# Optimization experiments

Measured on AMD Instinct MI355X. Metric: run time of the kernel, lower is better.

The kernel has to match this reference:

```python
import jax, jax.numpy as jnp
import numpy as np

D_MODEL = 1024
B, T_Q, T_KV = 4, 2048, 2048


def _linear_params(key, d_in, d_out):
    kw, kb = jax.random.split(key)
    W = jax.random.normal(kw, (d_out, d_in), dtype=jnp.float32) * 0.02
    b = jax.random.normal(kb, (d_out,), dtype=jnp.float32) * 0.02
    return W, b


def setup_inputs() -> dict:
    key = jax.random.key(0)
    ks = jax.random.split(key, 7)
    latent_space = jax.random.normal(ks[0], (B, T_Q, D_MODEL), dtype=jnp.float32)
    input_space = jax.random.normal(ks[1], (B, T_KV, D_MODEL), dtype=jnp.float32)
    Wl, bl = _linear_params(ks[2], D_MODEL, D_MODEL)
    Wu, bu = _linear_params(ks[3], D_MODEL, D_MODEL)
    WA, bA = _linear_params(ks[4], D_MODEL, D_MODEL)  # A_proj: d -> J (J = d)
    WV, bV = _linear_params(ks[5], D_MODEL, D_MODEL)  # V_proj: J -> d
    Wo, bo = _linear_params(ks[6], D_MODEL, D_MODEL)
    return {
        "latent_space": latent_space, "input_space": input_space,
        "Wl": Wl, "bl": bl, "Wu": Wu, "bu": bu,
        "WA": WA, "bA": bA, "WV": WV, "bV": bV,
        "Wo": Wo, "bo": bo,
    }


def reference(latent_space, input_space, Wl, bl, Wu, bu, WA, bA, WV, bV, Wo, bo):
    # emb_0 = l_proj(latent)            [B, T_q, d]
    emb0 = jnp.einsum('bqd,ed->bqe', latent_space, Wl) + bl
    # l = softmax(u_proj(emb_0), -1)^T  [B, d, T_q]
    l = jax.nn.softmax(jnp.einsum('bqd,ed->bqe', emb0, Wu) + bu, axis=-1)
    l = jnp.swapaxes(l, -2, -1)
    # D = A_proj(input)                 [B, T_kv, J]
    Dm = jnp.einsum('bkd,jd->bkj', input_space, WA) + bA
    # A = softmax(V_proj(D), dim=-2)    softmax over T_kv
    A = jax.nn.softmax(jnp.einsum('bkj,dj->bkd', Dm, WV) + bV, axis=-2)
    # w = A @ l                         [B, T_kv, T_q]
    w = jnp.einsum('bkd,bdq->bkq', A, l)
    # o = w @ o_proj(latent)            [B, T_kv, d]
    ov = jnp.einsum('bqd,ed->bqe', latent_space, Wo) + bo
    o = jnp.einsum('bkq,bqd->bkd', w, ov)
    return o
```

## Files before the change

### kernel.cpp

```cpp
#include <hip/hip_runtime.h>
#include <hip/hip_bf16.h>
#include <stdint.h>

typedef __attribute__((ext_vector_type(8))) short bf16x8;
typedef __attribute__((ext_vector_type(4))) float f32x4;
typedef __attribute__((ext_vector_type(4))) unsigned short u16x4;

#define B_  4
#define T_  2048
#define D_  1024
#define BM  128
#define BN  128
#define BK  32

__device__ __forceinline__ float bf2f(ushort u) {
  union { unsigned int i; float f; } v; v.i = ((unsigned int)u) << 16; return v.f;
}
__device__ __forceinline__ ushort f2bf(float f) {
  return (ushort)(__bfloat16_as_ushort(__float2bfloat16(f)));
}
__device__ __forceinline__ void async16(const void* g, void* l) {
  __builtin_amdgcn_global_load_lds(
      (const __attribute__((address_space(1))) void*)g,
      (__attribute__((address_space(3))) void*)l, 16, 0, 0);
}
__device__ __forceinline__ int swz4(int r) { return (r ^ (r >> 2)) & 3; }

__global__ __launch_bounds__(256)
void prep(const float* __restrict__ lat, const float* __restrict__ inp,
          const float* __restrict__ Wl, const float* __restrict__ bl,
          const float* __restrict__ Wu, const float* __restrict__ bu,
          const float* __restrict__ WA, const float* __restrict__ bA,
          const float* __restrict__ WV, const float* __restrict__ bV,
          const float* __restrict__ Wo, const float* __restrict__ bo,
          ushort* __restrict__ xBf, ushort* __restrict__ xBf2,
          ushort* __restrict__ w1, ushort* __restrict__ w2,
          ushort* __restrict__ wCatWo, float* __restrict__ bc, float* __restrict__ bc2)
{
  __shared__ alignas(16) ushort t[64 * 65];
  const long NW = (long)D_ * D_;
  const int bx = blockIdx.x;
  const int tid = threadIdx.x;
  if (bx < 16384) {
    const float* in = bx < 8192 ? lat : inp;
    ushort* out = bx < 8192 ? xBf : xBf2;
    const long i = (long)(bx & 8191) * 256 + tid;
    const float4 v = *(const float4*)(in + i * 4);
    u16x4 o;
    o[0] = f2bf(v.x); o[1] = f2bf(v.y); o[2] = f2bf(v.z); o[3] = f2bf(v.w);
    *(u16x4*)(out + i * 4) = o;
  } else if (bx < 19456) {
    const int seg = (bx - 16384) >> 10;
    const float* in  = seg == 0 ? Wu : (seg == 1 ? WV : Wo);
    ushort* out = seg == 0 ? w1 : (seg == 1 ? w1 + NW : wCatWo);
    const long i = (long)((bx - 16384) & 1023) * 256 + tid;
    const float4 v = *(const float4*)(in + i * 4);
    u16x4 o;
    o[0] = f2bf(v.x); o[1] = f2bf(v.y); o[2] = f2bf(v.z); o[3] = f2bf(v.w);
    *(u16x4*)(out + i * 4) = o;
  } else if (bx < 19968) {
    const int z = (bx - 19456) >> 8;
    const int w = (bx - 19456) & 255;
    const float* in = z ? WA : Wl;
    ushort* out = z ? w2 + NW : w2;
    const int c0 = (w & 15) * 64, r0 = (w >> 4) * 64;
    const int tx = tid & 15, ty = tid >> 4;
#pragma unroll
    for (int i = 0; i < 4; ++i) {
      const int r = ty + i * 16;
      const float4 v = *(const float4*)(in + (long)(r0 + r) * D_ + c0 + tx * 4);
      t[(tx * 4 + 0) * 65 + r] = f2bf(v.x);
      t[(tx * 4 + 1) * 65 + r] = f2bf(v.y);
      t[(tx * 4 + 2) * 65 + r] = f2bf(v.z);
      t[(tx * 4 + 3) * 65 + r] = f2bf(v.w);
    }
    __syncthreads();
#pragma unroll
    for (int i = 0; i < 4; ++i) {
      const int c = ty + i * 16;
      u16x4 v;
#pragma unroll
      for (int j = 0; j < 4; ++j) v[j] = t[c * 65 + tx * 4 + j];
      *(u16x4*)(out + (long)(c0 + c) * D_ + r0 + tx * 4) = v;
    }
  } else {
    const int z = (bx - 19968) >> 8;
    const int w = (bx - 19968) & 255;
    const float* W    = z ? WV : Wu;
    const float* bin  = z ? bA : bl;
    const float* badd = z ? bV : bu;
    float* out        = z ? bc2 : bc;
    const int wv = tid >> 6, lane = tid & 63;
    const int e = w * 4 + wv;
    const float* row = W + (long)e * D_;
    float s = 0.f;
#pragma unroll
    for (int i = 0; i < 16; ++i) s += row[lane + i * 64] * bin[lane + i * 64];
#pragma unroll
    for (int off = 32; off; off >>= 1) s += __shfl_xor(s, off);
    if (lane == 0) out[e] = s + badd[e];
  }
}

template<bool OUT_F32, bool HAS_BIAS, bool EXP_OUT>
__global__ __launch_bounds__(256, 2)
void gemm_nt(const ushort* __restrict__ A, const ushort* __restrict__ B,
             const float* __restrict__ bias, void* __restrict__ C,
             int N, int K, long sA, long sB, long sC)
{
  __shared__ alignas(16) ushort As[BM * BK];
  __shared__ alignas(16) ushort Bs[BN * BK];
  const int tid  = threadIdx.x;
  const int wave = tid >> 6;
  const int lane = tid & 63;
  const int wm   = wave >> 1;
  const int wn   = wave & 1;
  const int bz   = blockIdx.z;
  const int tileN = blockIdx.x * BN;
  const int tileM = blockIdx.y * BM;
  A += (long)bz * sA;
  B += (long)bz * sB;

  const int lrow   = lane >> 2;
  const int lchunk = (lane & 3) ^ swz4(lrow);

  f32x4 acc[4][4];
#pragma unroll
  for (int i = 0; i < 4; ++i)
#pragma unroll
    for (int j = 0; j < 4; ++j) acc[i][j] = (f32x4){0.f, 0.f, 0.f, 0.f};

  const int frow = lane & 15;
  const int kg   = lane >> 4;
  const int coff = ((kg ^ swz4(frow)) << 3);

  for (int kt = 0; kt < K; kt += BK) {
    __syncthreads();
#pragma unroll
    for (int i = 0; i < 2; ++i) {
      const int rg  = wave * 2 + i;
      const int row = rg * 16 + lrow;
      async16(A + (long)(tileM + row) * K + kt + lchunk * 8, (void*)(As + rg * 16 * BK));
      async16(B + (long)(tileN + row) * K + kt + lchunk * 8, (void*)(Bs + rg * 16 * BK));
    }
    __syncthreads();
    bf16x8 af[4], bfr[4];
#pragma unroll
    for (int mi = 0; mi < 4; ++mi)
      af[mi] = *(const bf16x8*)(As + (wm * 64 + mi * 16 + frow) * BK + coff);
#pragma unroll
    for (int ni = 0; ni < 4; ++ni)
      bfr[ni] = *(const bf16x8*)(Bs + (wn * 64 + ni * 16 + frow) * BK + coff);
#pragma unroll
    for (int mi = 0; mi < 4; ++mi)
#pragma unroll
      for (int ni = 0; ni < 4; ++ni)
        acc[mi][ni] = __builtin_amdgcn_mfma_f32_16x16x32_bf16(af[mi], bfr[ni], acc[mi][ni], 0, 0, 0);
  }

  const int rowbase = tileM + wm * 64 + ((lane >> 4) << 2);
  const int colbase = tileN + wn * 64 + (lane & 15);
#pragma unroll
  for (int ni = 0; ni < 4; ++ni) {
    const int col = colbase + ni * 16;
    float bv = 0.f;
    if constexpr (HAS_BIAS) bv = bias[col];
#pragma unroll
    for (int mi = 0; mi < 4; ++mi) {
#pragma unroll
      for (int r = 0; r < 4; ++r) {
        const int row = rowbase + mi * 16 + r;
        float v = acc[mi][ni][r] + bv;
        if constexpr (EXP_OUT) v = __expf(v);
        const long idx = (long)bz * sC + (long)row * N + col;
        if constexpr (OUT_F32) ((float*)C)[idx] = v;
        else ((ushort*)C)[idx] = f2bf(v);
      }
    }
  }
}

#define PH_SYNC_IN()                                               \
  __builtin_amdgcn_s_barrier();                                    \
  asm volatile("s_waitcnt lgkmcnt(0)" ::: "memory");               \
  __builtin_amdgcn_sched_barrier(0);                               \
  __builtin_amdgcn_s_setprio(1)
#define PH_SYNC_OUT()                                              \
  __builtin_amdgcn_s_setprio(0);                                   \
  __builtin_amdgcn_s_barrier()

__global__ __launch_bounds__(512, 2)
void gemm256(const ushort* __restrict__ A, const ushort* __restrict__ Bm,
             const float* __restrict__ bias1, const float* __restrict__ bias2,
             ushort* __restrict__ C1, ushort* __restrict__ C2,
             int ldA, int ldB)
{
  __shared__ alignas(16) ushort AbS[2 * 16384];
  __shared__ alignas(16) ushort BbS[2 * 16384];

  const int gx = gridDim.x;
  const int nwg = gx * gridDim.y;
  int fid = blockIdx.y * gx + blockIdx.x;
  fid = (fid & 7) * (nwg >> 3) + (fid >> 3);
  const int bx = fid % gx;
  const int by = fid / gx;
  const int tileM = by * 256, tileN = bx * 256;

  const int tid  = threadIdx.x;
  const int wid  = tid >> 6;
  const int lane = tid & 63;
  const int wm   = wid >> 2;
  const int wn   = wid & 3;

  const int srow = tid >> 2;
  const int sc   = (((tid & 3) ^ ((tid >> 3) & 3)) << 3);
  const ushort* gA0 = A  + (long)(tileM + srow) * ldA + sc;
  const ushort* gA1 = A  + (long)(tileM + 128 + srow) * ldA + sc;
  const ushort* gB0 = Bm + (long)(tileN + srow) * ldB + sc;
  const ushort* gB1 = Bm + (long)(tileN + 128 + srow) * ldB + sc;
  const int dofs = tid << 3;

#define STA(b, kh, t) { \
    async16(gA0 + (long)(t) * 64 + (kh) * 32, AbS + (b) * 16384 + (kh) * 8192 + dofs); \
    async16(gA1 + (long)(t) * 64 + (kh) * 32, AbS + (b) * 16384 + (kh) * 8192 + 4096 + dofs); }
#define STB(b, kh, t) { \
    async16(gB0 + (long)(t) * 64 + (kh) * 32, BbS + (b) * 16384 + (kh) * 8192 + dofs); \
    async16(gB1 + (long)(t) * 64 + (kh) * 32, BbS + (b) * 16384 + (kh) * 8192 + 4096 + dofs); }

  const int frow = lane & 15;
  const int cofs = (((lane >> 4) ^ ((frow >> 1) & 3)) << 3);
  int aoff[8], boff[4];
#pragma unroll
  for (int mi = 0; mi < 8; ++mi)
    aoff[mi] = wm * 4096 + (mi * 16 + frow) * 32 + cofs;
#pragma unroll
  for (int n = 0; n < 4; ++n) {
    const int Brow = wn * 64 + n * 16 + frow;
    boff[n] = (Brow >> 7) * 4096 + (Brow & 127) * 32 + cofs;
  }

  f32x4 acc[8][4];
#pragma unroll
  for (int i = 0; i < 8; ++i)
#pragma unroll
    for (int j = 0; j < 4; ++j) acc[i][j] = (f32x4){0.f, 0.f, 0.f, 0.f};

  STA(0, 0, 0); STB(0, 0, 0);
  STA(0, 1, 0); STB(0, 1, 0);
  STA(1, 0, 1); STB(1, 0, 1);
  asm volatile("s_waitcnt vmcnt(8)" ::: "memory");
  __builtin_amdgcn_s_barrier();

#pragma unroll 1
  for (int t = 0; t < 16; ++t) {
    const int buf = t & 1;
    const ushort* Ac = AbS + buf * 16384;
    const ushort* Bc = BbS + buf * 16384;
    bf16x8 fa[4], fb[4], ga[4];

#pragma unroll
    for (int n = 0; n < 4; ++n) fb[n] = *(const bf16x8*)(Bc + boff[n]);
#pragma unroll
    for (int m = 0; m < 4; ++m) fa[m] = *(const bf16x8*)(Ac + aoff[m]);
    if (t <= 14) { STA(buf ^ 1, 1, t + 1); STB(buf ^ 1, 1, t + 1); }
    PH_SYNC_IN();
#pragma unroll
    for (int m = 0; m < 4; ++m)
#pragma unroll
      for (int n = 0; n < 4; ++n)
        acc[m][n] = __builtin_amdgcn_mfma_f32_16x16x32_bf16(fa[m], fb[n], acc[m][n], 0, 0, 0);
    PH_SYNC_OUT();

#pragma unroll
    for (int m = 0; m < 4; ++m) ga[m] = *(const bf16x8*)(Ac + aoff[4 + m]);
    if (t <= 14) asm volatile("s_waitcnt vmcnt(8)" ::: "memory");
    else         asm volatile("s_waitcnt vmcnt(0)" ::: "memory");
    PH_SYNC_IN();
#pragma unroll
    for (int m = 0; m < 4; ++m)
#pragma unroll
      for (int n = 0; n < 4; ++n)
        acc[4 + m][n] = __builtin_amdgcn_mfma_f32_16x16x32_bf16(ga[m], fb[n], acc[4 + m][n], 0, 0, 0);
    PH_SYNC_OUT();

#pragma unroll
    for (int n = 0; n < 4; ++n) fb[n] = *(const bf16x8*)(Bc + boff[n] + 8192);
#pragma unroll
    for (int m = 0; m < 4; ++m) fa[m] = *(const bf16x8*)(Ac + aoff[m] + 8192);
    if (t <= 13) { STA(buf, 0, t + 2); STB(buf, 0, t + 2); }
    PH_SYNC_IN();
#pragma unroll
    for (int m = 0; m < 4; ++m)
#pragma unroll
      for (int n = 0; n < 4; ++n)
        acc[m][n] = __builtin_amdgcn_mfma_f32_16x16x32_bf16(fa[m], fb[n], acc[m][n], 0, 0, 0);
    PH_SYNC_OUT();

#pragma unroll
    for (int m = 0; m < 4; ++m) ga[m] = *(const bf16x8*)(Ac + aoff[4 + m] + 8192);
    if (t <= 13)      asm volatile("s_waitcnt vmcnt(8)" ::: "memory");
    else if (t == 14) asm volatile("s_waitcnt vmcnt(4)" ::: "memory");
    PH_SYNC_IN();
#pragma unroll
    for (int m = 0; m < 4; ++m)
#pragma unroll
      for (int n = 0; n < 4; ++n)
        acc[4 + m][n] = __builtin_amdgcn_mfma_f32_16x16x32_bf16(ga[m], fb[n], acc[4 + m][n], 0, 0, 0);
    PH_SYNC_OUT();
  }
#undef STA
#undef STB

  const bool second = tileN >= 1024;
  ushort* Cp = second ? C2 : C1;
  const float* bb = second ? bias2 : bias1;
  const int cb = tileN - (second ? 1024 : 0) + wn * 64 + (lane & 15);
  const int rb = tileM + wm * 128 + ((lane >> 4) << 2);
#pragma unroll
  for (int mi = 0; mi < 8; ++mi) {
    const int mrow = rb + mi * 16;
#pragma unroll
    for (int ni = 0; ni < 4; ++ni) {
      const int col = cb + ni * 16;
      const float bv = bb[col];
#pragma unroll
      for (int r = 0; r < 4; ++r)
        Cp[(long)(mrow + r) * 1024 + col] = f2bf(acc[mi][ni][r] + bv);
    }
  }
}

template<int MODE>
__global__ __launch_bounds__(512, 2)
void gemm128(const ushort* __restrict__ A, const ushort* __restrict__ Bm,
             const float* __restrict__ bias1, void* __restrict__ C1,
             int ldA, int ldB, long sAz, long sBz, long sCz)
{
  __shared__ alignas(16) ushort AbS[2 * 16384];
  __shared__ alignas(16) ushort BbS[2 * 8192];

  const int gx = gridDim.x, gy = gridDim.y;
  const int nwg = gx * gy * gridDim.z;
  int fid = (blockIdx.z * gy + blockIdx.y) * gx + blockIdx.x;
  fid = (fid & 7) * (nwg >> 3) + (fid >> 3);
  const int bx = fid % gx;
  const int by = (fid / gx) % gy;
  const int bz = fid / (gx * gy);
  const int tileM = by * 256, tileN = bx * 128;

  const ushort* Ap = A;
  const ushort* Bp = Bm;
  if constexpr (MODE == 2) {
    Ap += (long)(bz >> 1) * sAz + (long)(bz & 1) * 1024;
    Bp += (long)(bz >> 1) * sBz + (long)(bz & 1) * 1024;
  } else {
    Ap += (long)bz * sAz;
    Bp += (long)bz * sBz;
  }

  const int tid  = threadIdx.x;
  const int wid  = tid >> 6;
  const int lane = tid & 63;
  const int wm   = wid >> 1;
  const int wn   = wid & 1;

  const int srow = tid >> 2;
  const int sc   = (((tid & 3) ^ ((tid >> 3) & 3)) << 3);
  const ushort* gA0 = Ap + (long)(tileM + srow) * ldA + sc;
  const ushort* gA1 = Ap + (long)(tileM + 128 + srow) * ldA + sc;
  const ushort* gB0 = Bp + (long)(tileN + srow) * ldB + sc;
  const int dofs = tid << 3;

#define STA(b, kh, t) { \
    async16(gA0 + (long)(t) * 64 + (kh) * 32, AbS + (b) * 16384 + (kh) * 8192 + dofs); \
    async16(gA1 + (long)(t) * 64 + (kh) * 32, AbS + (b) * 16384 + (kh) * 8192 + 4096 + dofs); }
#define STB(b, kh, t) \
    async16(gB0 + (long)(t) * 64 + (kh) * 32, BbS + (b) * 8192 + (kh) * 4096 + dofs);

  const int frow = lane & 15;
  const int cofs = (((lane >> 4) ^ ((frow >> 1) & 3)) << 3);
  int aoff[4], boff[4];
#pragma unroll
  for (int mi = 0; mi < 4; ++mi) {
    const int R = wm * 64 + mi * 16 + frow;
    aoff[mi] = (R >> 7) * 4096 + (R & 127) * 32 + cofs;
  }
#pragma unroll
  for (int n = 0; n < 4; ++n)
    boff[n] = (wn * 64 + n * 16 + frow) * 32 + cofs;

  f32x4 acc[4][4];
#pragma unroll
  for (int i = 0; i < 4; ++i)
#pragma unroll
    for (int j = 0; j < 4; ++j) acc[i][j] = (f32x4){0.f, 0.f, 0.f, 0.f};

  STA(0, 0, 0); STB(0, 0, 0);
  STA(0, 1, 0); STB(0, 1, 0);
  STA(1, 0, 1); STB(1, 0, 1);
  asm volatile("s_waitcnt vmcnt(6)" ::: "memory");
  __builtin_amdgcn_s_barrier();

#pragma unroll 1
  for (int t = 0; t < 16; ++t) {
    const int buf = t & 1;
    const ushort* Ac = AbS + buf * 16384;
    const ushort* Bc = BbS + buf * 8192;
    bf16x8 fa[4], fb[4];

#pragma unroll
    for (int n = 0; n < 4; ++n) fb[n] = *(const bf16x8*)(Bc + boff[n]);
#pragma unroll
    for (int m = 0; m < 4; ++m) fa[m] = *(const bf16x8*)(Ac + aoff[m]);
    if (t <= 14) { STA(buf ^ 1, 1, t + 1); STB(buf ^ 1, 1, t + 1); }
    if (t <= 14) asm volatile("s_waitcnt vmcnt(6)" ::: "memory");
    else         asm volatile("s_waitcnt vmcnt(0)" ::: "memory");
    PH_SYNC_IN();
#pragma unroll
    for (int m = 0; m < 4; ++m)
#pragma unroll
      for (int n = 0; n < 4; ++n)
        acc[m][n] = __builtin_amdgcn_mfma_f32_16x16x32_bf16(fa[m], fb[n], acc[m][n], 0, 0, 0);
    PH_SYNC_OUT();

#pragma unroll
    for (int n = 0; n < 4; ++n) fb[n] = *(const bf16x8*)(Bc + boff[n] + 4096);
#pragma unroll
    for (int m = 0; m < 4; ++m) fa[m] = *(const bf16x8*)(Ac + aoff[m] + 8192);
    if (t <= 13) { STA(buf, 0, t + 2); STB(buf, 0, t + 2); }
    if (t <= 13)      asm volatile("s_waitcnt vmcnt(6)" ::: "memory");
    else if (t == 14) asm volatile("s_waitcnt vmcnt(3)" ::: "memory");
    PH_SYNC_IN();
#pragma unroll
    for (int m = 0; m < 4; ++m)
#pragma unroll
      for (int n = 0; n < 4; ++n)
        acc[m][n] = __builtin_amdgcn_mfma_f32_16x16x32_bf16(fa[m], fb[n], acc[m][n], 0, 0, 0);
    PH_SYNC_OUT();
  }
#undef STA
#undef STB

  const int cb = tileN + wn * 64 + (lane & 15);
  const int rb = tileM + wm * 64 + ((lane >> 4) << 2);

  if constexpr (MODE == 1) {
    ushort* Cp = (ushort*)C1;
#pragma unroll
    for (int ni = 0; ni < 4; ++ni) {
      const int col = cb + ni * 16;
      const float bv = bias1[col];
#pragma unroll
      for (int mi = 0; mi < 4; ++mi)
#pragma unroll
        for (int r = 0; r < 4; ++r)
          Cp[(long)(rb + mi * 16 + r) * 1024 + col] = f2bf(__expf(acc[mi][ni][r] + bv));
    }
  } else if constexpr (MODE == 2) {
    ushort* Cp = (ushort*)C1 + ((long)(bz & 1) * B_ + (bz >> 1)) * ((long)D_ * D_);
#pragma unroll
    for (int ni = 0; ni < 4; ++ni) {
      const int col = cb + ni * 16;
#pragma unroll
      for (int mi = 0; mi < 4; ++mi)
#pragma unroll
        for (int r = 0; r < 4; ++r)
          Cp[(long)(rb + mi * 16 + r) * 1024 + col] = f2bf(acc[mi][ni][r]);
    }
  } else {
    float* Cp = (float*)C1 + (long)bz * sCz;
#pragma unroll
    for (int ni = 0; ni < 4; ++ni) {
      const int col = cb + ni * 16;
#pragma unroll
      for (int mi = 0; mi < 4; ++mi)
#pragma unroll
        for (int r = 0; r < 4; ++r)
          Cp[(long)(rb + mi * 16 + r) * 1024 + col] = acc[mi][ni][r];
    }
  }
}

__global__ __launch_bounds__(256)
void reduce2_scale(const ushort* __restrict__ P, const float* __restrict__ cinv,
                   ushort* __restrict__ MT)
{
  const long stride = (long)B_ * D_ * D_;
  const long base = ((long)blockIdx.x * 256 + threadIdx.x) * 8;
  const int b = (int)(base >> 20);
  const int e0 = (int)(base & (D_ - 1));
  bf16x8 p0 = *(const bf16x8*)(P + base);
  bf16x8 p1 = *(const bf16x8*)(P + stride + base);
  const float4 c0 = *(const float4*)(cinv + (long)b * D_ + e0);
  const float4 c1 = *(const float4*)(cinv + (long)b * D_ + e0 + 4);
  const float cc[8] = {c0.x, c0.y, c0.z, c0.w, c1.x, c1.y, c1.z, c1.w};
  bf16x8 o;
#pragma unroll
  for (int j = 0; j < 8; ++j)
    o[j] = (short)f2bf((bf2f((ushort)p0[j]) + bf2f((ushort)p1[j])) * cc[j]);
  *(bf16x8*)(MT + base) = o;
}

__global__ __launch_bounds__(256)
void softmax_row(ushort* __restrict__ S)
{
  const long base = (long)blockIdx.x * D_;
  const int tid = threadIdx.x;
  float e[4], s = 0.f;
#pragma unroll
  for (int i = 0; i < 4; ++i) { e[i] = __expf(bf2f(S[base + i * 256 + tid])); s += e[i]; }
#pragma unroll
  for (int off = 32; off; off >>= 1) s += __shfl_xor(s, off);
  __shared__ float reds[4];
  if ((tid & 63) == 0) reds[tid >> 6] = s;
  __syncthreads();
  s = reds[0] + reds[1] + reds[2] + reds[3];
  const float inv = 1.f / s;
#pragma unroll
  for (int i = 0; i < 4; ++i)
    S[base + i * 256 + tid] = f2bf(e[i] * inv);
}

__global__ __launch_bounds__(256)
void transpose2(const ushort* __restrict__ l, ushort* __restrict__ lT,
                const ushort* __restrict__ ov, ushort* __restrict__ ovT)
{
  __shared__ alignas(16) ushort t[64 * 65];
  const int z = blockIdx.z;
  const int b = z & (B_ - 1);
  const ushort* in = (z < B_ ? l : ov) + (long)b * T_ * D_;
  ushort* out      = (z < B_ ? lT : ovT) + (long)b * (long)D_ * T_;
  const int c0 = blockIdx.x * 64, r0 = blockIdx.y * 64;
  const int tx = threadIdx.x & 15, ty = threadIdx.x >> 4;
#pragma unroll
  for (int i = 0; i < 4; ++i) {
    const int r = ty + i * 16;
    u16x4 v = *(const u16x4*)(in + (long)(r0 + r) * D_ + c0 + tx * 4);
#pragma unroll
    for (int c = 0; c < 4; ++c) t[(tx * 4 + c) * 65 + r] = v[c];
  }
  __syncthreads();
#pragma unroll
  for (int i = 0; i < 4; ++i) {
    const int c = ty + i * 16;
    u16x4 v;
#pragma unroll
    for (int j = 0; j < 4; ++j) v[j] = t[c * 65 + tx * 4 + j];
    *(u16x4*)(out + (long)(c0 + c) * T_ + r0 + tx * 4) = v;
  }
}

__global__ __launch_bounds__(256)
void colsum_part(const ushort* __restrict__ E, float* __restrict__ psum)
{
  const int d = blockIdx.x * 256 + threadIdx.x;
  const int c = blockIdx.y;
  const int b = blockIdx.z;
  const ushort* p = E + ((long)b * T_ + (long)c * 128) * D_ + d;
  float s = 0.f;
#pragma unroll 4
  for (int r = 0; r < 128; ++r) s += bf2f(p[(long)r * D_]);
  psum[((long)b * 16 + c) * D_ + d] = s;
}

__global__ __launch_bounds__(256)
void colsum_comb(const float* __restrict__ psum, float* __restrict__ cinv)
{
  const int d = blockIdx.x * 256 + threadIdx.x;
  const int b = blockIdx.y;
  float s = 0.f;
#pragma unroll
  for (int c = 0; c < 16; ++c) s += psum[((long)b * 16 + c) * D_ + d];
  cinv[(long)b * D_ + d] = 1.f / s;
}

extern "C" void kernel_launch(void* const* d_in, const int* in_sizes, int n_in,
                              void* d_out, int out_size, void* d_ws, size_t ws_size,
                              hipStream_t stream)
{
  (void)in_sizes; (void)n_in; (void)out_size; (void)ws_size;
  const float* lat = (const float*)d_in[0];
  const float* inp = (const float*)d_in[1];
  const float* Wl  = (const float*)d_in[2];
  const float* bl  = (const float*)d_in[3];
  const float* Wu  = (const float*)d_in[4];
  const float* bu  = (const float*)d_in[5];
  const float* WA  = (const float*)d_in[6];
  const float* bA  = (const float*)d_in[7];
  const float* WV  = (const float*)d_in[8];
  const float* bV  = (const float*)d_in[9];
  const float* Wo  = (const float*)d_in[10];
  const float* bo  = (const float*)d_in[11];

  char* w = (char*)d_ws;
  auto carve = [&](size_t bytes) { char* p = w; w += (bytes + 255) & ~(size_t)255; return p; };
  const long NT = (long)B_ * T_ * D_;
  const long NW = (long)D_ * D_;
  ushort* xBf   = (ushort*)carve(NT * 2);
  ushort* xBf2  = (ushort*)carve(NT * 2);
  ushort* bufA  = (ushort*)carve(NT * 2);
  ushort* bufB  = (ushort*)carve(NT * 2);
  ushort* scr   = (ushort*)carve(NT * 2);
  ushort* MT    = (ushort*)carve((long)B_ * NW * 2);
  ushort* wCat  = (ushort*)carve(3 * NW * 2);
  float*  bc    = (float*)carve(D_ * 4);
  float*  bc2   = (float*)carve(D_ * 4);
  float*  psum  = (float*)carve(64 * 1024 * 4);
  float*  cinv  = (float*)carve(8 * 1024 * 4);
  ushort* w1 = scr;
  ushort* w2 = scr + 2 * NW;
  ushort* ovT = scr;
  ushort* part = bufB;

  const dim3 blk(256, 1, 1);
  const dim3 blk5(512, 1, 1);

  prep<<<dim3(20480), blk, 0, stream>>>(lat, inp, Wl, bl, Wu, bu, WA, bA, WV, bV, Wo, bo,
                                        xBf, xBf2, w1, w2, wCat + NW, bc, bc2);
  gemm_nt<false, false, false><<<dim3(8, 8, 2), blk, 0, stream>>>(
      w1, w2, nullptr, wCat, D_, D_, NW, NW, 2 * NW);
  gemm256<<<dim3(8, 32, 1), blk5, 0, stream>>>(
      xBf, wCat, bc, bo, bufB, bufA, D_, D_);
  softmax_row<<<dim3(B_ * T_), blk, 0, stream>>>(bufB);
  transpose2<<<dim3(16, 32, 2 * B_), blk, 0, stream>>>(bufB, xBf, bufA, ovT);
  gemm128<2><<<dim3(8, 4, 8), blk5, 0, stream>>>(
      ovT, xBf, nullptr, part, T_, T_, (long)D_ * T_, (long)D_ * T_, 0);
  gemm128<1><<<dim3(8, 32, 1), blk5, 0, stream>>>(
      xBf2, wCat + 2 * NW, bc2, bufA, D_, D_, 0, 0, 0);
  colsum_part<<<dim3(4, 16, B_), blk, 0, stream>>>(bufA, psum);
  colsum_comb<<<dim3(4, B_, 1), blk, 0, stream>>>(psum, cinv);
  reduce2_scale<<<dim3(2048), blk, 0, stream>>>(part, cinv, MT);
  gemm128<3><<<dim3(8, 8, 4), blk5, 0, stream>>>(
      bufA, MT, nullptr, d_out, D_, D_,
      (long)T_ * D_, NW, (long)T_ * D_);
}
```

Baseline: 321.2 us.

## Use BK=64 swizzled tiles with triple-buffered LDS pipelines and drop gemm_nt

Both pipelined GEMM kernels now load full 64-wide K tiles per row with an 8-way XOR swizzle instead of two 32-wide halves. Their LDS buffering moves to a triple-buffer rotation (B only in gemm256, A and B in gemm128), so prefetches are issued two tiles ahead and spread across the phases. The old simple gemm_nt used for weight fusion is replaced by a new MODE 0 of the pipelined gemm128. This is meant to improve global-load width and latency hiding, at the cost of more LDS per block, which may lower occupancy.

```diff
diff --git a/kernel.cpp b/kernel.cpp
--- a/kernel.cpp
+++ b/kernel.cpp
@@ -9,9 +9,6 @@
 #define B_  4
 #define T_  2048
 #define D_  1024
-#define BM  128
-#define BN  128
-#define BK  32
 
 __device__ __forceinline__ float bf2f(ushort u) {
   union { unsigned int i; float f; } v; v.i = ((unsigned int)u) << 16; return v.f;
@@ -24,7 +21,6 @@
       (const __attribute__((address_space(1))) void*)g,
       (__attribute__((address_space(3))) void*)l, 16, 0, 0);
 }
-__device__ __forceinline__ int swz4(int r) { return (r ^ (r >> 2)) & 3; }
 
 __global__ __launch_bounds__(256)
 void prep(const float* __restrict__ lat, const float* __restrict__ inp,
@@ -102,84 +98,6 @@
   }
 }
 
-template<bool OUT_F32, bool HAS_BIAS, bool EXP_OUT>
-__global__ __launch_bounds__(256, 2)
-void gemm_nt(const ushort* __restrict__ A, const ushort* __restrict__ B,
-             const float* __restrict__ bias, void* __restrict__ C,
-             int N, int K, long sA, long sB, long sC)
-{
-  __shared__ alignas(16) ushort As[BM * BK];
-  __shared__ alignas(16) ushort Bs[BN * BK];
-  const int tid  = threadIdx.x;
-  const int wave = tid >> 6;
-  const int lane = tid & 63;
-  const int wm   = wave >> 1;
-  const int wn   = wave & 1;
-  const int bz   = blockIdx.z;
-  const int tileN = blockIdx.x * BN;
-  const int tileM = blockIdx.y * BM;
-  A += (long)bz * sA;
-  B += (long)bz * sB;
-
-  const int lrow   = lane >> 2;
-  const int lchunk = (lane & 3) ^ swz4(lrow);
-
-  f32x4 acc[4][4];
-#pragma unroll
-  for (int i = 0; i < 4; ++i)
-#pragma unroll
-    for (int j = 0; j < 4; ++j) acc[i][j] = (f32x4){0.f, 0.f, 0.f, 0.f};
-
-  const int frow = lane & 15;
-  const int kg   = lane >> 4;
-  const int coff = ((kg ^ swz4(frow)) << 3);
-
-  for (int kt = 0; kt < K; kt += BK) {
-    __syncthreads();
-#pragma unroll
-    for (int i = 0; i < 2; ++i) {
-      const int rg  = wave * 2 + i;
-      const int row = rg * 16 + lrow;
-      async16(A + (long)(tileM + row) * K + kt + lchunk * 8, (void*)(As + rg * 16 * BK));
-      async16(B + (long)(tileN + row) * K + kt + lchunk * 8, (void*)(Bs + rg * 16 * BK));
-    }
-    __syncthreads();
-    bf16x8 af[4], bfr[4];
-#pragma unroll
-    for (int mi = 0; mi < 4; ++mi)
-      af[mi] = *(const bf16x8*)(As + (wm * 64 + mi * 16 + frow) * BK + coff);
-#pragma unroll
-    for (int ni = 0; ni < 4; ++ni)
-      bfr[ni] = *(const bf16x8*)(Bs + (wn * 64 + ni * 16 + frow) * BK + coff);
-#pragma unroll
-    for (int mi = 0; mi < 4; ++mi)
-#pragma unroll
-      for (int ni = 0; ni < 4; ++ni)
-        acc[mi][ni] = __builtin_amdgcn_mfma_f32_16x16x32_bf16(af[mi], bfr[ni], acc[mi][ni], 0, 0, 0);
-  }
-
-  const int rowbase = tileM + wm * 64 + ((lane >> 4) << 2);
-  const int colbase = tileN + wn * 64 + (lane & 15);
-#pragma unroll
-  for (int ni = 0; ni < 4; ++ni) {
-    const int col = colbase + ni * 16;
-    float bv = 0.f;
-    if constexpr (HAS_BIAS) bv = bias[col];
-#pragma unroll
-    for (int mi = 0; mi < 4; ++mi) {
-#pragma unroll
-      for (int r = 0; r < 4; ++r) {
-        const int row = rowbase + mi * 16 + r;
-        float v = acc[mi][ni][r] + bv;
-        if constexpr (EXP_OUT) v = __expf(v);
-        const long idx = (long)bz * sC + (long)row * N + col;
-        if constexpr (OUT_F32) ((float*)C)[idx] = v;
-        else ((ushort*)C)[idx] = f2bf(v);
-      }
-    }
-  }
-}
-
 #define PH_SYNC_IN()                                               \
   __builtin_amdgcn_s_barrier();                                    \
   asm volatile("s_waitcnt lgkmcnt(0)" ::: "memory");               \
@@ -189,6 +107,7 @@
   __builtin_amdgcn_s_setprio(0);                                   \
   __builtin_amdgcn_s_barrier()
 
+
 __global__ __launch_bounds__(512, 2)
 void gemm256(const ushort* __restrict__ A, const ushort* __restrict__ Bm,
              const float* __restrict__ bias1, const float* __restrict__ bias2,
@@ -196,7 +115,7 @@
              int ldA, int ldB)
 {
   __shared__ alignas(16) ushort AbS[2 * 16384];
-  __shared__ alignas(16) ushort BbS[2 * 16384];
+  __shared__ alignas(16) ushort BbS[3 * 16384];
 
   const int gx = gridDim.x;
   const int nwg = gx * gridDim.y;
@@ -212,32 +131,26 @@
   const int wm   = wid >> 2;
   const int wn   = wid & 3;
 
-  const int srow = tid >> 2;
-  const int sc   = (((tid & 3) ^ ((tid >> 3) & 3)) << 3);
-  const ushort* gA0 = A  + (long)(tileM + srow) * ldA + sc;
-  const ushort* gA1 = A  + (long)(tileM + 128 + srow) * ldA + sc;
-  const ushort* gB0 = Bm + (long)(tileN + srow) * ldB + sc;
-  const ushort* gB1 = Bm + (long)(tileN + 128 + srow) * ldB + sc;
-  const int dofs = tid << 3;
-
-#define STA(b, kh, t) { \
-    async16(gA0 + (long)(t) * 64 + (kh) * 32, AbS + (b) * 16384 + (kh) * 8192 + dofs); \
-    async16(gA1 + (long)(t) * 64 + (kh) * 32, AbS + (b) * 16384 + (kh) * 8192 + 4096 + dofs); }
-#define STB(b, kh, t) { \
-    async16(gB0 + (long)(t) * 64 + (kh) * 32, BbS + (b) * 16384 + (kh) * 8192 + dofs); \
-    async16(gB1 + (long)(t) * 64 + (kh) * 32, BbS + (b) * 16384 + (kh) * 8192 + 4096 + dofs); }
+  const int srow8 = tid >> 3;
+  const int scol8 = ((tid & 7) ^ (srow8 & 7)) << 3;
+  const ushort* gAs = A  + (long)(tileM + srow8) * ldA + scol8;
+  const ushort* gBs = Bm + (long)(tileN + srow8) * ldB + scol8;
+  const int sdst = tid << 3;
+
+#define STA(b, i, t) async16(gAs + (long)((i) * 64) * ldA + (t) * 64, \
+                             AbS + (b) * 16384 + (i) * 4096 + sdst)
+#define STB(b, i, t) async16(gBs + (long)((i) * 64) * ldB + (t) * 64, \
+                             BbS + (b) * 16384 + (i) * 4096 + sdst)
 
   const int frow = lane & 15;
-  const int cofs = (((lane >> 4) ^ ((frow >> 1) & 3)) << 3);
-  int aoff[8], boff[4];
-#pragma unroll
-  for (int mi = 0; mi < 8; ++mi)
-    aoff[mi] = wm * 4096 + (mi * 16 + frow) * 32 + cofs;
-#pragma unroll
-  for (int n = 0; n < 4; ++n) {
-    const int Brow = wn * 64 + n * 16 + frow;
-    boff[n] = (Brow >> 7) * 4096 + (Brow & 127) * 32 + cofs;
-  }
+  const int kg   = lane >> 4;
+  const int ck0 = ((kg       ^ (frow & 7)) << 3);
+  const int ck1 = (((4 + kg) ^ (frow & 7)) << 3);
+  int aoffr[8], boffr[4];
+#pragma unroll
+  for (int mi = 0; mi < 8; ++mi) aoffr[mi] = (wm * 128 + mi * 16 + frow) * 64;
+#pragma unroll
+  for (int n = 0; n < 4; ++n)    boffr[n]  = (wn * 64 + n * 16 + frow) * 64;
 
   f32x4 acc[8][4];
 #pragma unroll
@@ -245,24 +158,32 @@
 #pragma unroll
     for (int j = 0; j < 4; ++j) acc[i][j] = (f32x4){0.f, 0.f, 0.f, 0.f};
 
-  STA(0, 0, 0); STB(0, 0, 0);
-  STA(0, 1, 0); STB(0, 1, 0);
-  STA(1, 0, 1); STB(1, 0, 1);
+#pragma unroll
+  for (int i = 0; i < 4; ++i) STA(0, i, 0);
+#pragma unroll
+  for (int i = 0; i < 4; ++i) STB(0, i, 0);
+#pragma unroll
+  for (int i = 0; i < 4; ++i) STA(1, i, 1);
+#pragma unroll
+  for (int i = 0; i < 4; ++i) STB(1, i, 1);
   asm volatile("s_waitcnt vmcnt(8)" ::: "memory");
   __builtin_amdgcn_s_barrier();
 
 #pragma unroll 1
   for (int t = 0; t < 16; ++t) {
     const int buf = t & 1;
+    const int bB  = t - (t / 3) * 3;
+    const int nA  = (t + 1) & 1;
+    const int nB  = (t + 2) - ((t + 2) / 3) * 3;
     const ushort* Ac = AbS + buf * 16384;
-    const ushort* Bc = BbS + buf * 16384;
+    const ushort* Bc = BbS + bB * 16384;
     bf16x8 fa[4], fb[4], ga[4];
 
 #pragma unroll
-    for (int n = 0; n < 4; ++n) fb[n] = *(const bf16x8*)(Bc + boff[n]);
-#pragma unroll
-    for (int m = 0; m < 4; ++m) fa[m] = *(const bf16x8*)(Ac + aoff[m]);
-    if (t <= 14) { STA(buf ^ 1, 1, t + 1); STB(buf ^ 1, 1, t + 1); }
+    for (int n = 0; n < 4; ++n) fb[n] = *(const bf16x8*)(Bc + boffr[n] + ck0);
+#pragma unroll
+    for (int m = 0; m < 4; ++m) fa[m] = *(const bf16x8*)(Ac + aoffr[m] + ck0);
+    if (t >= 1 && t <= 14) { STA(nA, 0, t + 1); STA(nA, 1, t + 1); }
     PH_SYNC_IN();
 #pragma unroll
     for (int m = 0; m < 4; ++m)
@@ -272,9 +193,9 @@
     PH_SYNC_OUT();
 
 #pragma unroll
-    for (int m = 0; m < 4; ++m) ga[m] = *(const bf16x8*)(Ac + aoff[4 + m]);
-    if (t <= 14) asm volatile("s_waitcnt vmcnt(8)" ::: "memory");
-    else         asm volatile("s_waitcnt vmcnt(0)" ::: "memory");
+    for (int m = 0; m < 4; ++m) ga[m] = *(const bf16x8*)(Ac + aoffr[4 + m] + ck0);
+    if (t >= 1 && t <= 14) { STA(nA, 2, t + 1); STA(nA, 3, t + 1); }
+    if (t <= 13)           { STB(nB, 0, t + 2); STB(nB, 1, t + 2); }
     PH_SYNC_IN();
 #pragma unroll
     for (int m = 0; m < 4; ++m)
@@ -284,10 +205,10 @@
     PH_SYNC_OUT();
 
 #pragma unroll
-    for (int n = 0; n < 4; ++n) fb[n] = *(const bf16x8*)(Bc + boff[n] + 8192);
-#pragma unroll
-    for (int m = 0; m < 4; ++m) fa[m] = *(const bf16x8*)(Ac + aoff[m] + 8192);
-    if (t <= 13) { STA(buf, 0, t + 2); STB(buf, 0, t + 2); }
+    for (int n = 0; n < 4; ++n) fb[n] = *(const bf16x8*)(Bc + boffr[n] + ck1);
+#pragma unroll
+    for (int m = 0; m < 4; ++m) fa[m] = *(const bf16x8*)(Ac + aoffr[m] + ck1);
+    if (t <= 13) { STB(nB, 2, t + 2); STB(nB, 3, t + 2); }
     PH_SYNC_IN();
 #pragma unroll
     for (int m = 0; m < 4; ++m)
@@ -297,9 +218,9 @@
     PH_SYNC_OUT();
 
 #pragma unroll
-    for (int m = 0; m < 4; ++m) ga[m] = *(const bf16x8*)(Ac + aoff[4 + m] + 8192);
-    if (t <= 13)      asm volatile("s_waitcnt vmcnt(8)" ::: "memory");
-    else if (t == 14) asm volatile("s_waitcnt vmcnt(4)" ::: "memory");
+    for (int m = 0; m < 4; ++m) ga[m] = *(const bf16x8*)(Ac + aoffr[4 + m] + ck1);
+    if (t <= 13)      { asm volatile("s_waitcnt vmcnt(4)" ::: "memory"); }
+    else if (t == 14) { asm volatile("s_waitcnt vmcnt(0)" ::: "memory"); }
     PH_SYNC_IN();
 #pragma unroll
     for (int m = 0; m < 4; ++m)
@@ -336,8 +257,8 @@
              const float* __restrict__ bias1, void* __restrict__ C1,
              int ldA, int ldB, long sAz, long sBz, long sCz)
 {
-  __shared__ alignas(16) ushort AbS[2 * 16384];
-  __shared__ alignas(16) ushort BbS[2 * 8192];
+  __shared__ alignas(16) ushort AbS[3 * 16384];
+  __shared__ alignas(16) ushort BbS[3 * 8192];
 
   const int gx = gridDim.x, gy = gridDim.y;
   const int nwg = gx * gy * gridDim.z;
@@ -364,30 +285,26 @@
   const int wm   = wid >> 1;
   const int wn   = wid & 1;
 
-  const int srow = tid >> 2;
-  const int sc   = (((tid & 3) ^ ((tid >> 3) & 3)) << 3);
-  const ushort* gA0 = Ap + (long)(tileM + srow) * ldA + sc;
-  const ushort* gA1 = Ap + (long)(tileM + 128 + srow) * ldA + sc;
-  const ushort* gB0 = Bp + (long)(tileN + srow) * ldB + sc;
-  const int dofs = tid << 3;
-
-#define STA(b, kh, t) { \
-    async16(gA0 + (long)(t) * 64 + (kh) * 32, AbS + (b) * 16384 + (kh) * 8192 + dofs); \
-    async16(gA1 + (long)(t) * 64 + (kh) * 32, AbS + (b) * 16384 + (kh) * 8192 + 4096 + dofs); }
-#define STB(b, kh, t) \
-    async16(gB0 + (long)(t) * 64 + (kh) * 32, BbS + (b) * 8192 + (kh) * 4096 + dofs);
+  const int srow8 = tid >> 3;
+  const int scol8 = ((tid & 7) ^ (srow8 & 7)) << 3;
+  const ushort* gAs = Ap + (long)(tileM + srow8) * ldA + scol8;
+  const ushort* gBs = Bp + (long)(tileN + srow8) * ldB + scol8;
+  const int sdst = tid << 3;
+
+#define STA(b, i, t) async16(gAs + (long)((i) * 64) * ldA + (t) * 64, \
+                             AbS + (b) * 16384 + (i) * 4096 + sdst)
+#define STB(b, i, t) async16(gBs + (long)((i) * 64) * ldB + (t) * 64, \
+                             BbS + (b) * 8192 + (i) * 4096 + sdst)
 
   const int frow = lane & 15;
-  const int cofs = (((lane >> 4) ^ ((frow >> 1) & 3)) << 3);
-  int aoff[4], boff[4];
-#pragma unroll
-  for (int mi = 0; mi < 4; ++mi) {
-    const int R = wm * 64 + mi * 16 + frow;
-    aoff[mi] = (R >> 7) * 4096 + (R & 127) * 32 + cofs;
-  }
-#pragma unroll
-  for (int n = 0; n < 4; ++n)
-    boff[n] = (wn * 64 + n * 16 + frow) * 32 + cofs;
+  const int kg   = lane >> 4;
+  const int ck0 = ((kg       ^ (frow & 7)) << 3);
+  const int ck1 = (((4 + kg) ^ (frow & 7)) << 3);
+  int aoffr[4], boffr[4];
+#pragma unroll
+  for (int mi = 0; mi < 4; ++mi) aoffr[mi] = (wm * 64 + mi * 16 + frow) * 64;
+#pragma unroll
+  for (int n = 0; n < 4; ++n)    boffr[n]  = (wn * 64 + n * 16 + frow) * 64;
 
   f32x4 acc[4][4];
 #pragma unroll
@@ -395,26 +312,28 @@
 #pragma unroll
     for (int j = 0; j < 4; ++j) acc[i][j] = (f32x4){0.f, 0.f, 0.f, 0.f};
 
-  STA(0, 0, 0); STB(0, 0, 0);
-  STA(0, 1, 0); STB(0, 1, 0);
-  STA(1, 0, 1); STB(1, 0, 1);
+#pragma unroll
+  for (int i = 0; i < 4; ++i) STA(0, i, 0);
+  STB(0, 0, 0); STB(0, 1, 0);
+#pragma unroll
+  for (int i = 0; i < 4; ++i) STA(1, i, 1);
+  STB(1, 0, 1); STB(1, 1, 1);
   asm volatile("s_waitcnt vmcnt(6)" ::: "memory");
   __builtin_amdgcn_s_barrier();
 
 #pragma unroll 1
   for (int t = 0; t < 16; ++t) {
-    const int buf = t & 1;
-    const ushort* Ac = AbS + buf * 16384;
-    const ushort* Bc = BbS + buf * 8192;
+    const int bufT = t - (t / 3) * 3;
+    const int nb   = (t + 2) - ((t + 2) / 3) * 3;
+    const ushort* Ac = AbS + bufT * 16384;
+    const ushort* Bc = BbS + bufT * 8192;
     bf16x8 fa[4], fb[4];
 
 #pragma unroll
-    for (int n = 0; n < 4; ++n) fb[n] = *(const bf16x8*)(Bc + boff[n]);
-#pragma unroll
-    for (int m = 0; m < 4; ++m) fa[m] = *(const bf16x8*)(Ac + aoff[m]);
-    if (t <= 14) { STA(buf ^ 1, 1, t + 1); STB(buf ^ 1, 1, t + 1); }
-    if (t <= 14) asm volatile("s_waitcnt vmcnt(6)" ::: "memory");
-    else         asm volatile("s_waitcnt vmcnt(0)" ::: "memory");
+    for (int n = 0; n < 4; ++n) fb[n] = *(const bf16x8*)(Bc + boffr[n] + ck0);
+#pragma unroll
+    for (int m = 0; m < 4; ++m) fa[m] = *(const bf16x8*)(Ac + aoffr[m] + ck0);
+    if (t <= 13) { STA(nb, 0, t + 2); STA(nb, 1, t + 2); STA(nb, 2, t + 2); STA(nb, 3, t + 2); }
     PH_SYNC_IN();
 #pragma unroll
     for (int m = 0; m < 4; ++m)
@@ -424,12 +343,12 @@
     PH_SYNC_OUT();
 
 #pragma unroll
-    for (int n = 0; n < 4; ++n) fb[n] = *(const bf16x8*)(Bc + boff[n] + 4096);
-#pragma unroll
-    for (int m = 0; m < 4; ++m) fa[m] = *(const bf16x8*)(Ac + aoff[m] + 8192);
-    if (t <= 13) { STA(buf, 0, t + 2); STB(buf, 0, t + 2); }
-    if (t <= 13)      asm volatile("s_waitcnt vmcnt(6)" ::: "memory");
-    else if (t == 14) asm volatile("s_waitcnt vmcnt(3)" ::: "memory");
+    for (int n = 0; n < 4; ++n) fb[n] = *(const bf16x8*)(Bc + boffr[n] + ck1);
+#pragma unroll
+    for (int m = 0; m < 4; ++m) fa[m] = *(const bf16x8*)(Ac + aoffr[m] + ck1);
+    if (t <= 13) { STB(nb, 0, t + 2); STB(nb, 1, t + 2); }
+    if (t <= 13)      { asm volatile("s_waitcnt vmcnt(6)" ::: "memory"); }
+    else if (t == 14) { asm volatile("s_waitcnt vmcnt(0)" ::: "memory"); }
     PH_SYNC_IN();
 #pragma unroll
     for (int m = 0; m < 4; ++m)
@@ -444,7 +363,18 @@
   const int cb = tileN + wn * 64 + (lane & 15);
   const int rb = tileM + wm * 64 + ((lane >> 4) << 2);
 
-  if constexpr (MODE == 1) {
+  if constexpr (MODE == 0) {
+    ushort* Cp = (ushort*)C1 + (long)bz * sCz;
+#pragma unroll
+    for (int ni = 0; ni < 4; ++ni) {
+      const int col = cb + ni * 16;
+#pragma unroll
+      for (int mi = 0; mi < 4; ++mi)
+#pragma unroll
+        for (int r = 0; r < 4; ++r)
+          Cp[(long)(rb + mi * 16 + r) * 1024 + col] = f2bf(acc[mi][ni][r]);
+    }
+  } else if constexpr (MODE == 1) {
     ushort* Cp = (ushort*)C1;
 #pragma unroll
     for (int ni = 0; ni < 4; ++ni) {
@@ -617,7 +547,7 @@
 
   prep<<<dim3(20480), blk, 0, stream>>>(lat, inp, Wl, bl, Wu, bu, WA, bA, WV, bV, Wo, bo,
                                         xBf, xBf2, w1, w2, wCat + NW, bc, bc2);
-  gemm_nt<false, false, false><<<dim3(8, 8, 2), blk, 0, stream>>>(
+  gemm128<0><<<dim3(8, 4, 2), blk5, 0, stream>>>(
       w1, w2, nullptr, wCat, D_, D_, NW, NW, 2 * NW);
   gemm256<<<dim3(8, 32, 1), blk5, 0, stream>>>(
       xBf, wCat, bc, bo, bufB, bufA, D_, D_);
```

Measured after the change: 309.6 us. -3.6%, faster.
